# Kernel tuning notes

Measured on AMD Instinct MI355X. Metric: run time of the kernel, lower is better.

Reference implementation:

```python
import jax, jax.numpy as jnp
import numpy as np

B, H, W = 128, 64, 64
MAP = 128          # gff mapping_dim
GFF_SCALE = 10.0   # common default scale for Gaussian Fourier features


def _ku(k, shape, fan_in):
    # torch kaiming_uniform_(a=sqrt(5)) -> bound = 1/sqrt(fan_in)
    b = 1.0 / np.sqrt(fan_in)
    return jax.random.uniform(k, shape, jnp.float32, -b, b)


def setup_inputs() -> dict:
    key = jax.random.key(0)
    ks = jax.random.split(key, 16)
    coords = jax.random.uniform(ks[0], (B, 2, H, W), jnp.float32)
    Bmat = GFF_SCALE * jax.random.normal(ks[1], (2, MAP), jnp.float32)
    # FMMLinear(256, 256_out? no) -- linear1: in=256, out=256, rank=70
    L1 = _ku(ks[2], (256, 70), 70)
    R1 = _ku(ks[3], (70, 256), 256)
    b1 = jax.random.uniform(ks[4], (256,), jnp.float32, -1/np.sqrt(256), 1/np.sqrt(256))
    # linear2: in=256, out=128, rank=10
    L2 = _ku(ks[5], (128, 10), 10)
    R2 = _ku(ks[6], (10, 256), 256)
    b2 = jax.random.uniform(ks[7], (128,), jnp.float32, -1/np.sqrt(256), 1/np.sqrt(256))
    # dense layers (torch nn.Linear default init)
    W3 = _ku(ks[8], (32, 128), 128)
    b3 = jax.random.uniform(ks[9], (32,), jnp.float32, -1/np.sqrt(128), 1/np.sqrt(128))
    W4 = _ku(ks[10], (16, 32), 32)
    b4 = jax.random.uniform(ks[11], (16,), jnp.float32, -1/np.sqrt(32), 1/np.sqrt(32))
    W5 = _ku(ks[12], (3, 16), 16)
    b5 = jax.random.uniform(ks[13], (3,), jnp.float32, -1/np.sqrt(16), 1/np.sqrt(16))
    return dict(coords=coords, Bmat=Bmat, L1=L1, R1=R1, b1=b1,
                L2=L2, R2=R2, b2=b2, W3=W3, b3=b3, W4=W4, b4=b4, W5=W5, b5=b5)


def reference(coords, Bmat, L1, R1, b1, L2, R2, b2, W3, b3, W4, b4, W5, b5):
    # Gaussian Fourier features: [B,2,H,W] -> [B,H,W,2*MAP]
    proj = (2.0 * jnp.pi) * jnp.einsum('bchw,cm->bhwm', coords, Bmat)
    x = jnp.concatenate([jnp.sin(proj), jnp.cos(proj)], axis=-1)
    x = x.reshape(-1, 2 * MAP)                       # (b h w) c
    x = jax.nn.relu(x @ (L1 @ R1).T + b1)            # FMM linear1
    x = jax.nn.relu(x @ (L2 @ R2).T + b2)            # FMM linear2
    x = jax.nn.relu(x @ W3.T + b3)
    x = jax.nn.relu(x @ W4.T + b4)
    out = (x @ W5.T + b5)[None]                      # [1, B*H*W, 3]
    return out
```

## Files before the change

kernel.cpp:

```cpp
#include <hip/hip_runtime.h>


typedef __attribute__((ext_vector_type(8))) short bf16x8;
typedef __attribute__((ext_vector_type(4))) float f32x4;
typedef __attribute__((ext_vector_type(4))) int i32x4;

#define LFENCE() asm volatile("s_waitcnt lgkmcnt(0)" ::: "memory")

__device__ inline unsigned short f2bf(float f) {
  unsigned u = __float_as_uint(f);
  return (unsigned short)((u + 0x7FFFu + ((u >> 16) & 1u)) >> 16);
}

#if __has_builtin(__builtin_amdgcn_cvt_pk_bf16_f32)
typedef __attribute__((ext_vector_type(2))) __bf16 bf16x2;
__device__ inline unsigned pk2bf(float a, float b) {
  bf16x2 v = __builtin_amdgcn_cvt_pk_bf16_f32(a, b);
  return __builtin_bit_cast(unsigned, v);
}
#else
__device__ inline unsigned pk2bf(float a, float b) {
  return ((__float_as_uint(a) + 0x8000u) >> 16) |
         ((__float_as_uint(b) + 0x8000u) & 0xFFFF0000u);
}
#endif

__global__ __launch_bounds__(256) void prep_pack(
    const float* __restrict__ R1, const float* __restrict__ L1,
    const float* __restrict__ R2, const float* __restrict__ L2,
    const float* __restrict__ W3, const float* __restrict__ W4,
    void* __restrict__ ws) {
  unsigned short* w16 = (unsigned short*)ws;
  float* wf = (float*)ws;
  int e = blockIdx.x * 256 + threadIdx.x;
  if (e < 20480) {
    int kt = e / 2560, rem = e % 2560;
    int n = rem >> 5, oj = rem & 31;
    int k = kt * 32 + oj;
    int feat = (k & 1) ? 128 + (k >> 1) : (k >> 1);
    w16[e] = f2bf((n < 70) ? R1[n * 256 + feat] : 0.0f);
  } else if (e < 45056) {
    int f = e - 20480;
    int kt = f / 8192, rem = f % 8192;
    int n = rem >> 5, oj = rem & 31;
    int r = kt * 32 + (oj & 1) * 16 + (oj >> 1);
    w16[e] = f2bf((r < 70) ? L1[n * 70 + r] : 0.0f);
  } else if (e < 49152) {
    int g = e - 45056;
    int rd = g / 512, rem = g % 512;
    int n = rem >> 5, oj = rem & 31;
    int j = rd * 32 + (oj & 1) * 16 + (oj >> 1);
    w16[e] = f2bf((n < 10) ? R2[n * 256 + j] : 0.0f);
  } else if (e < 53248) {
    int f = e - 49152;
    int j = f & 7, h = (f >> 3) & 3, n = (f >> 5) & 15, nt = f >> 9;
    int k = h * 8 + j;
    w16[e] = f2bf((k < 10) ? L2[(nt * 16 + n) * 10 + k] : 0.0f);
  } else if (e < 57344) {
    int f = e - 53248;
    int oj = f & 31, n = (f >> 5) & 15, nt2 = (f >> 9) & 1, rd = f >> 10;
    int i = rd * 32 + (oj & 1) * 16 + (oj >> 1);
    w16[e] = f2bf(W3[(nt2 * 16 + n) * 128 + i]);
  } else if (e < 57856) {
    int h2 = e - 57344;
    int q = h2 >> 4, p = h2 & 15;
    wf[28672 + h2] = W4[p * 32 + q];
  }
}

__global__ __launch_bounds__(128, 2) void mlp_mfma(
    const float* __restrict__ coords, const float* __restrict__ Bm,
    const float* __restrict__ b1, const float* __restrict__ b2,
    const float* __restrict__ b3v, const float* __restrict__ b4v,
    const float* __restrict__ W5, const float* __restrict__ b5,
    const void* __restrict__ ws, float* __restrict__ out) {
  const int l = threadIdx.x & 63;
  const int wv = threadIdx.x >> 6;
  const int lo = l & 15, hi = l >> 4;
  const int pix0 = blockIdx.x * 128 + wv * 64;

  __shared__ __align__(16) char smem[20480];
  char* slice = smem + wv * 10240;
  unsigned short* Y16 = (unsigned short*)slice;
  unsigned short* X16 = (unsigned short*)slice;
  float* O3f = (float*)slice;

  const unsigned short* R1p = (const unsigned short*)ws;
  const unsigned short* L1p = ((const unsigned short*)ws) + 20480;
  const unsigned short* R2p = ((const unsigned short*)ws) + 45056;
  const unsigned short* L2p = ((const unsigned short*)ws) + 49152;
  const unsigned short* W3p = ((const unsigned short*)ws) + 53248;
  const float* W4T = ((const float*)ws) + 28672;

  const f32x4 fz = {0.0f, 0.0f, 0.0f, 0.0f};

  float c0m[4], c1m[4];
#pragma unroll
  for (int mt = 0; mt < 4; ++mt) {
    int p = pix0 + mt * 16 + lo;
    int bb = p >> 12, hw = p & 4095;
    c0m[mt] = coords[bb * 8192 + hw];
    c1m[mt] = coords[bb * 8192 + 4096 + hw];
  }

  f32x4 y[4][5];
#pragma unroll
  for (int mt = 0; mt < 4; ++mt)
#pragma unroll
    for (int nt = 0; nt < 5; ++nt) y[mt][nt] = fz;

  float bm0[4], bm1[4];
#pragma unroll
  for (int p = 0; p < 4; ++p) {
    int m = hi * 4 + p;
    bm0[p] = Bm[m]; bm1[p] = Bm[128 + m];
  }
  for (int kt = 0; kt < 8; ++kt) {
    float nb0[4], nb1[4];
    if (kt < 7) {
#pragma unroll
      for (int p = 0; p < 4; ++p) {
        int m = (kt + 1) * 16 + hi * 4 + p;
        nb0[p] = Bm[m]; nb1[p] = Bm[128 + m];
      }
    }
    bf16x8 bfr[5];
#pragma unroll
    for (int nt = 0; nt < 5; ++nt)
      bfr[nt] = *(const bf16x8*)(R1p + ((kt * 80 + nt * 16 + lo) * 4 + hi) * 8);
    bf16x8 af[4];
#pragma unroll
    for (int mt = 0; mt < 4; ++mt) {
#pragma unroll
      for (int p = 0; p < 4; ++p) {
        float u = fmaf(c0m[mt], bm0[p], c1m[mt] * bm1[p]);
        float t = u - floorf(u);
        float s = __builtin_amdgcn_sinf(t);
        float c = __builtin_amdgcn_cosf(t);
        ((unsigned*)&af[mt])[p] = pk2bf(s, c);
      }
    }
#pragma unroll
    for (int mt = 0; mt < 4; ++mt)
#pragma unroll
      for (int nt = 0; nt < 5; ++nt)
        y[mt][nt] = __builtin_amdgcn_mfma_f32_16x16x32_bf16(af[mt], bfr[nt],
                                                            y[mt][nt], 0, 0, 0);
#pragma unroll
    for (int p = 0; p < 4; ++p) { bm0[p] = nb0[p]; bm1[p] = nb1[p]; }
  }

#pragma unroll
  for (int mt = 0; mt < 4; ++mt)
#pragma unroll
    for (int r = 0; r < 4; ++r) {
      int row = mt * 16 + hi * 4 + r;
      *(unsigned*)(Y16 + row * 72 + lo * 2)      = pk2bf(y[mt][0][r], y[mt][1][r]);
      *(unsigned*)(Y16 + row * 72 + 32 + lo * 2) = pk2bf(y[mt][2][r], y[mt][3][r]);
    }
  LFENCE();
  bf16x8 ay[4][3];
#pragma unroll
  for (int mt = 0; mt < 4; ++mt)
#pragma unroll
    for (int kt = 0; kt < 2; ++kt)
      ay[mt][kt] = *(const bf16x8*)(Y16 + (mt * 16 + lo) * 72 + kt * 32 + hi * 8);
  LFENCE();
#pragma unroll
  for (int mt = 0; mt < 4; ++mt)
#pragma unroll
    for (int r = 0; r < 4; ++r) {
      int row = mt * 16 + hi * 4 + r;
      *(unsigned*)(Y16 + row * 72 + lo * 2) = pk2bf(y[mt][4][r], 0.0f);
    }
  LFENCE();
#pragma unroll
  for (int mt = 0; mt < 4; ++mt)
    ay[mt][2] = *(const bf16x8*)(Y16 + (mt * 16 + lo) * 72 + hi * 8);
  LFENCE();

  f32x4 zfr[4];
#pragma unroll
  for (int mt = 0; mt < 4; ++mt) zfr[mt] = fz;

#pragma unroll
  for (int rd = 0; rd < 8; ++rd) {
    unsigned short* Xb = X16 + (rd & 1) * 2560;
    bf16x8 blE[3], blO[3];
#pragma unroll
    for (int kt = 0; kt < 3; ++kt) {
      blE[kt] = *(const bf16x8*)(L1p + ((kt * 256 + (2 * rd) * 16 + lo) * 4 + hi) * 8);
      blO[kt] = *(const bf16x8*)(L1p + ((kt * 256 + (2 * rd + 1) * 16 + lo) * 4 + hi) * 8);
    }
    float biasE = b1[2 * rd * 16 + lo];
    float biasO = b1[(2 * rd + 1) * 16 + lo];
    f32x4 cfE[4], cfO[4];
#pragma unroll
    for (int mt = 0; mt < 4; ++mt) { cfE[mt] = fz; cfO[mt] = fz; }
#pragma unroll
    for (int kt = 0; kt < 3; ++kt)
#pragma unroll
      for (int mt = 0; mt < 4; ++mt) {
        cfE[mt] = __builtin_amdgcn_mfma_f32_16x16x32_bf16(ay[mt][kt], blE[kt],
                                                          cfE[mt], 0, 0, 0);
        cfO[mt] = __builtin_amdgcn_mfma_f32_16x16x32_bf16(ay[mt][kt], blO[kt],
                                                          cfO[mt], 0, 0, 0);
      }
#pragma unroll
    for (int mt = 0; mt < 4; ++mt)
#pragma unroll
      for (int r = 0; r < 4; ++r) {
        float v0 = fmaxf(cfE[mt][r] + biasE, 0.0f);
        float v1 = fmaxf(cfO[mt][r] + biasO, 0.0f);
        *(unsigned*)(Xb + (mt * 16 + hi * 4 + r) * 40 + lo * 2) = pk2bf(v0, v1);
      }
    LFENCE();
    bf16x8 br = *(const bf16x8*)(R2p + (rd * 16 + lo) * 32 + hi * 8);
#pragma unroll
    for (int mt = 0; mt < 4; ++mt) {
      bf16x8 aa = *(const bf16x8*)(Xb + (mt * 16 + lo) * 40 + hi * 8);
      zfr[mt] = __builtin_amdgcn_mfma_f32_16x16x32_bf16(aa, br, zfr[mt], 0, 0, 0);
    }
  }

  unsigned short* Z16 = X16;
#pragma unroll
  for (int mt = 0; mt < 4; ++mt)
#pragma unroll
    for (int r = 0; r < 4; ++r)
      Z16[(mt * 16 + hi * 4 + r) * 40 + lo] =
          (unsigned short)(pk2bf(zfr[mt][r], 0.0f) & 0xFFFFu);
  *(i32x4*)(Z16 + l * 40 + 16) = (i32x4){0, 0, 0, 0};
  *(i32x4*)(Z16 + l * 40 + 24) = (i32x4){0, 0, 0, 0};
  LFENCE();
  bf16x8 az[4];
#pragma unroll
  for (int mt = 0; mt < 4; ++mt)
    az[mt] = *(const bf16x8*)(Z16 + (mt * 16 + lo) * 40 + hi * 8);
  LFENCE();

  f32x4 o3fr[4][2];
#pragma unroll
  for (int mt = 0; mt < 4; ++mt) { o3fr[mt][0] = fz; o3fr[mt][1] = fz; }

#pragma unroll
  for (int rd = 0; rd < 4; ++rd) {
    unsigned short* Xb = X16 + (rd & 1) * 2560;
    bf16x8 wlE = *(const bf16x8*)(L2p + ((2 * rd) * 16 + lo) * 32 + hi * 8);
    bf16x8 wlO = *(const bf16x8*)(L2p + ((2 * rd + 1) * 16 + lo) * 32 + hi * 8);
    float biasE = b2[2 * rd * 16 + lo];
    float biasO = b2[(2 * rd + 1) * 16 + lo];
    f32x4 cfE[4], cfO[4];
#pragma unroll
    for (int mt = 0; mt < 4; ++mt) {
      cfE[mt] = __builtin_amdgcn_mfma_f32_16x16x32_bf16(az[mt], wlE, fz, 0, 0, 0);
      cfO[mt] = __builtin_amdgcn_mfma_f32_16x16x32_bf16(az[mt], wlO, fz, 0, 0, 0);
    }
#pragma unroll
    for (int mt = 0; mt < 4; ++mt)
#pragma unroll
      for (int r = 0; r < 4; ++r) {
        float v0 = fmaxf(cfE[mt][r] + biasE, 0.0f);
        float v1 = fmaxf(cfO[mt][r] + biasO, 0.0f);
        *(unsigned*)(Xb + (mt * 16 + hi * 4 + r) * 40 + lo * 2) = pk2bf(v0, v1);
      }
    LFENCE();
    bf16x8 bw0 = *(const bf16x8*)(W3p + ((rd * 2 + 0) * 16 + lo) * 32 + hi * 8);
    bf16x8 bw1 = *(const bf16x8*)(W3p + ((rd * 2 + 1) * 16 + lo) * 32 + hi * 8);
#pragma unroll
    for (int mt = 0; mt < 4; ++mt) {
      bf16x8 aa = *(const bf16x8*)(Xb + (mt * 16 + lo) * 40 + hi * 8);
      o3fr[mt][0] = __builtin_amdgcn_mfma_f32_16x16x32_bf16(aa, bw0, o3fr[mt][0],
                                                            0, 0, 0);
      o3fr[mt][1] = __builtin_amdgcn_mfma_f32_16x16x32_bf16(aa, bw1, o3fr[mt][1],
                                                            0, 0, 0);
    }
  }

  LFENCE();
#pragma unroll
  for (int mt = 0; mt < 4; ++mt)
#pragma unroll
    for (int nt2 = 0; nt2 < 2; ++nt2)
#pragma unroll
      for (int r = 0; r < 4; ++r)
        O3f[(mt * 16 + hi * 4 + r) * 33 + nt2 * 16 + lo] =
            fmaxf(o3fr[mt][nt2][r] + b3v[nt2 * 16 + lo], 0.0f);
  LFENCE();

  float o3l[32];
#pragma unroll
  for (int q = 0; q < 32; ++q) o3l[q] = O3f[l * 33 + q];

  float o4[16];
#pragma unroll
  for (int p = 0; p < 16; ++p) o4[p] = b4v[p];
#pragma unroll
  for (int q = 0; q < 32; ++q) {
    float a = o3l[q];
    const float* __restrict__ w4 = W4T + q * 16;
#pragma unroll
    for (int p = 0; p < 16; ++p) o4[p] = fmaf(a, w4[p], o4[p]);
  }
#pragma unroll
  for (int p = 0; p < 16; ++p) o4[p] = fmaxf(o4[p], 0.0f);

#pragma unroll
  for (int e = 0; e < 3; ++e) {
    float acc = b5[e];
    const float* __restrict__ w5 = W5 + e * 16;
#pragma unroll
    for (int p = 0; p < 16; ++p) acc = fmaf(o4[p], w5[p], acc);
    out[(pix0 + l) * 3 + e] = acc;
  }
}

extern "C" void kernel_launch(void* const* d_in, const int* in_sizes, int n_in,
                              void* d_out, int out_size, void* d_ws, size_t ws_size,
                              hipStream_t stream) {
  const float* coords = (const float*)d_in[0];
  const float* Bmat   = (const float*)d_in[1];
  const float* L1     = (const float*)d_in[2];
  const float* R1     = (const float*)d_in[3];
  const float* b1     = (const float*)d_in[4];
  const float* L2     = (const float*)d_in[5];
  const float* R2     = (const float*)d_in[6];
  const float* b2     = (const float*)d_in[7];
  const float* W3     = (const float*)d_in[8];
  const float* b3     = (const float*)d_in[9];
  const float* W4     = (const float*)d_in[10];
  const float* b4     = (const float*)d_in[11];
  const float* W5     = (const float*)d_in[12];
  const float* b5     = (const float*)d_in[13];

  prep_pack<<<227, 256, 0, stream>>>(R1, L1, R2, L2, W3, W4, d_ws);
  mlp_mfma<<<4096, 128, 0, stream>>>(coords, Bmat, b1, b2, b3, b4, W5, b5,
                                     d_ws, (float*)d_out);
}
```

Baseline: 184.9 us.

## Software-pipeline MFMA layer chains, move W4 layer to MFMA, use single-wave blocks

Changes the kernel to one 64-thread wave per block, with more blocks and a smaller shared buffer. The linear1→R2 and L2→W3 chains are software-pipelined: weight fragments and biases for the next round are prefetched, and the previous round's MFMA is issued alongside the current round's. The Y tile is written once with a wider padded stride, which removes one LDS round trip. The fp32 scalar W4 layer becomes a bf16 MFMA fed from a new packed W4 layout, trading some precision and adding register pressure.

```diff
diff --git a/kernel.cpp b/kernel.cpp
--- a/kernel.cpp
+++ b/kernel.cpp
@@ -31,7 +31,6 @@
     const float* __restrict__ W3, const float* __restrict__ W4,
     void* __restrict__ ws) {
   unsigned short* w16 = (unsigned short*)ws;
-  float* wf = (float*)ws;
   int e = blockIdx.x * 256 + threadIdx.x;
   if (e < 20480) {
     int kt = e / 2560, rem = e % 2560;
@@ -53,44 +52,42 @@
     w16[e] = f2bf((n < 10) ? R2[n * 256 + j] : 0.0f);
   } else if (e < 53248) {
     int f = e - 49152;
-    int j = f & 7, h = (f >> 3) & 3, n = (f >> 5) & 15, nt = f >> 9;
-    int k = h * 8 + j;
+    int k = f & 31, n = (f >> 5) & 15, nt = f >> 9;
     w16[e] = f2bf((k < 10) ? L2[(nt * 16 + n) * 10 + k] : 0.0f);
   } else if (e < 57344) {
     int f = e - 53248;
-    int oj = f & 31, n = (f >> 5) & 15, nt2 = (f >> 9) & 1, rd = f >> 10;
+    int oj = f & 31, n = (f >> 5) & 15, s = (f >> 9) & 1, rd = f >> 10;
     int i = rd * 32 + (oj & 1) * 16 + (oj >> 1);
-    w16[e] = f2bf(W3[(nt2 * 16 + n) * 128 + i]);
+    w16[e] = f2bf(W3[(s * 16 + n) * 128 + i]);
   } else if (e < 57856) {
-    int h2 = e - 57344;
-    int q = h2 >> 4, p = h2 & 15;
-    wf[28672 + h2] = W4[p * 32 + q];
-  }
-}
-
-__global__ __launch_bounds__(128, 2) void mlp_mfma(
+    int f = e - 57344;
+    int n = f >> 5, oj = f & 31;
+    int q = (oj & 1) * 16 + (oj >> 1);
+    w16[e] = f2bf(W4[n * 32 + q]);
+  }
+}
+
+__global__ __launch_bounds__(64, 2) void mlp_mfma(
     const float* __restrict__ coords, const float* __restrict__ Bm,
     const float* __restrict__ b1, const float* __restrict__ b2,
     const float* __restrict__ b3v, const float* __restrict__ b4v,
     const float* __restrict__ W5, const float* __restrict__ b5,
     const void* __restrict__ ws, float* __restrict__ out) {
-  const int l = threadIdx.x & 63;
-  const int wv = threadIdx.x >> 6;
+  const int l = threadIdx.x;
   const int lo = l & 15, hi = l >> 4;
-  const int pix0 = blockIdx.x * 128 + wv * 64;
-
-  __shared__ __align__(16) char smem[20480];
-  char* slice = smem + wv * 10240;
-  unsigned short* Y16 = (unsigned short*)slice;
-  unsigned short* X16 = (unsigned short*)slice;
-  float* O3f = (float*)slice;
+  const int pix0 = blockIdx.x * 64;
+
+  __shared__ __align__(16) char smem[13312];
+  unsigned short* Y16 = (unsigned short*)smem;
+  unsigned short* X16 = (unsigned short*)smem;
+  float* O4f = (float*)smem;
 
   const unsigned short* R1p = (const unsigned short*)ws;
   const unsigned short* L1p = ((const unsigned short*)ws) + 20480;
   const unsigned short* R2p = ((const unsigned short*)ws) + 45056;
   const unsigned short* L2p = ((const unsigned short*)ws) + 49152;
   const unsigned short* W3p = ((const unsigned short*)ws) + 53248;
-  const float* W4T = ((const float*)ws) + 28672;
+  const unsigned short* W4p = ((const unsigned short*)ws) + 57344;
 
   const f32x4 fz = {0.0f, 0.0f, 0.0f, 0.0f};
 
@@ -127,7 +124,7 @@
     bf16x8 bfr[5];
 #pragma unroll
     for (int nt = 0; nt < 5; ++nt)
-      bfr[nt] = *(const bf16x8*)(R1p + ((kt * 80 + nt * 16 + lo) * 4 + hi) * 8);
+      bfr[nt] = *(const bf16x8*)(R1p + (kt * 80 + nt * 16 + lo) * 32 + hi * 8);
     bf16x8 af[4];
 #pragma unroll
     for (int mt = 0; mt < 4; ++mt) {
@@ -155,71 +152,84 @@
 #pragma unroll
     for (int r = 0; r < 4; ++r) {
       int row = mt * 16 + hi * 4 + r;
-      *(unsigned*)(Y16 + row * 72 + lo * 2)      = pk2bf(y[mt][0][r], y[mt][1][r]);
-      *(unsigned*)(Y16 + row * 72 + 32 + lo * 2) = pk2bf(y[mt][2][r], y[mt][3][r]);
-    }
+      *(unsigned*)(Y16 + row * 104 + lo * 2)      = pk2bf(y[mt][0][r], y[mt][1][r]);
+      *(unsigned*)(Y16 + row * 104 + 32 + lo * 2) = pk2bf(y[mt][2][r], y[mt][3][r]);
+      *(unsigned*)(Y16 + row * 104 + 64 + lo * 2) = pk2bf(y[mt][4][r], 0.0f);
+    }
+
+  bf16x8 WE[3], WO[3], WEn[3], WOn[3];
+#pragma unroll
+  for (int kt = 0; kt < 3; ++kt) {
+    WE[kt] = *(const bf16x8*)(L1p + (kt * 256 + lo) * 32 + hi * 8);
+    WO[kt] = *(const bf16x8*)(L1p + (kt * 256 + 16 + lo) * 32 + hi * 8);
+  }
+  float bE = b1[lo], bO = b1[16 + lo], bEn, bOn;
+  bf16x8 br_c = *(const bf16x8*)(R2p + lo * 32 + hi * 8);
+  bf16x8 br_u, br_n;
+
   LFENCE();
   bf16x8 ay[4][3];
 #pragma unroll
   for (int mt = 0; mt < 4; ++mt)
 #pragma unroll
-    for (int kt = 0; kt < 2; ++kt)
-      ay[mt][kt] = *(const bf16x8*)(Y16 + (mt * 16 + lo) * 72 + kt * 32 + hi * 8);
-  LFENCE();
-#pragma unroll
-  for (int mt = 0; mt < 4; ++mt)
-#pragma unroll
-    for (int r = 0; r < 4; ++r) {
-      int row = mt * 16 + hi * 4 + r;
-      *(unsigned*)(Y16 + row * 72 + lo * 2) = pk2bf(y[mt][4][r], 0.0f);
-    }
-  LFENCE();
-#pragma unroll
-  for (int mt = 0; mt < 4; ++mt)
-    ay[mt][2] = *(const bf16x8*)(Y16 + (mt * 16 + lo) * 72 + hi * 8);
-  LFENCE();
+    for (int kt = 0; kt < 3; ++kt)
+      ay[mt][kt] = *(const bf16x8*)(Y16 + (mt * 16 + lo) * 104 + kt * 32 + hi * 8);
 
   f32x4 zfr[4];
 #pragma unroll
   for (int mt = 0; mt < 4; ++mt) zfr[mt] = fz;
-
-#pragma unroll
-  for (int rd = 0; rd < 8; ++rd) {
-    unsigned short* Xb = X16 + (rd & 1) * 2560;
-    bf16x8 blE[3], blO[3];
-#pragma unroll
-    for (int kt = 0; kt < 3; ++kt) {
-      blE[kt] = *(const bf16x8*)(L1p + ((kt * 256 + (2 * rd) * 16 + lo) * 4 + hi) * 8);
-      blO[kt] = *(const bf16x8*)(L1p + ((kt * 256 + (2 * rd + 1) * 16 + lo) * 4 + hi) * 8);
-    }
-    float biasE = b1[2 * rd * 16 + lo];
-    float biasO = b1[(2 * rd + 1) * 16 + lo];
+  bf16x8 aa[4];
+
+#pragma unroll
+  for (int rd = 0; rd <= 8; ++rd) {
     f32x4 cfE[4], cfO[4];
-#pragma unroll
-    for (int mt = 0; mt < 4; ++mt) { cfE[mt] = fz; cfO[mt] = fz; }
-#pragma unroll
-    for (int kt = 0; kt < 3; ++kt)
-#pragma unroll
-      for (int mt = 0; mt < 4; ++mt) {
-        cfE[mt] = __builtin_amdgcn_mfma_f32_16x16x32_bf16(ay[mt][kt], blE[kt],
-                                                          cfE[mt], 0, 0, 0);
-        cfO[mt] = __builtin_amdgcn_mfma_f32_16x16x32_bf16(ay[mt][kt], blO[kt],
-                                                          cfO[mt], 0, 0, 0);
-      }
-#pragma unroll
-    for (int mt = 0; mt < 4; ++mt)
-#pragma unroll
-      for (int r = 0; r < 4; ++r) {
-        float v0 = fmaxf(cfE[mt][r] + biasE, 0.0f);
-        float v1 = fmaxf(cfO[mt][r] + biasO, 0.0f);
-        *(unsigned*)(Xb + (mt * 16 + hi * 4 + r) * 40 + lo * 2) = pk2bf(v0, v1);
-      }
-    LFENCE();
-    bf16x8 br = *(const bf16x8*)(R2p + (rd * 16 + lo) * 32 + hi * 8);
-#pragma unroll
-    for (int mt = 0; mt < 4; ++mt) {
-      bf16x8 aa = *(const bf16x8*)(Xb + (mt * 16 + lo) * 40 + hi * 8);
-      zfr[mt] = __builtin_amdgcn_mfma_f32_16x16x32_bf16(aa, br, zfr[mt], 0, 0, 0);
+    if (rd < 8) {
+#pragma unroll
+      for (int mt = 0; mt < 4; ++mt) { cfE[mt] = fz; cfO[mt] = fz; }
+#pragma unroll
+      for (int kt = 0; kt < 3; ++kt)
+#pragma unroll
+        for (int mt = 0; mt < 4; ++mt) {
+          cfE[mt] = __builtin_amdgcn_mfma_f32_16x16x32_bf16(ay[mt][kt], WE[kt],
+                                                            cfE[mt], 0, 0, 0);
+          cfO[mt] = __builtin_amdgcn_mfma_f32_16x16x32_bf16(ay[mt][kt], WO[kt],
+                                                            cfO[mt], 0, 0, 0);
+        }
+    }
+    if (rd > 0) {
+#pragma unroll
+      for (int mt = 0; mt < 4; ++mt)
+        zfr[mt] = __builtin_amdgcn_mfma_f32_16x16x32_bf16(aa[mt], br_u,
+                                                          zfr[mt], 0, 0, 0);
+    }
+    if (rd < 8) {
+      unsigned short* Xb = X16 + (rd & 1) * 2560;
+#pragma unroll
+      for (int mt = 0; mt < 4; ++mt)
+#pragma unroll
+        for (int r = 0; r < 4; ++r) {
+          float v0 = fmaxf(cfE[mt][r] + bE, 0.0f);
+          float v1 = fmaxf(cfO[mt][r] + bO, 0.0f);
+          *(unsigned*)(Xb + (mt * 16 + hi * 4 + r) * 40 + lo * 2) = pk2bf(v0, v1);
+        }
+      if (rd < 7) {
+#pragma unroll
+        for (int kt = 0; kt < 3; ++kt) {
+          WEn[kt] = *(const bf16x8*)(L1p + (kt * 256 + (2 * rd + 2) * 16 + lo) * 32 + hi * 8);
+          WOn[kt] = *(const bf16x8*)(L1p + (kt * 256 + (2 * rd + 3) * 16 + lo) * 32 + hi * 8);
+        }
+        bEn = b1[(2 * rd + 2) * 16 + lo];
+        bOn = b1[(2 * rd + 3) * 16 + lo];
+        br_n = *(const bf16x8*)(R2p + ((rd + 1) * 16 + lo) * 32 + hi * 8);
+      }
+      LFENCE();
+#pragma unroll
+      for (int mt = 0; mt < 4; ++mt)
+        aa[mt] = *(const bf16x8*)(Xb + (mt * 16 + lo) * 40 + hi * 8);
+      br_u = br_c; br_c = br_n;
+#pragma unroll
+      for (int kt = 0; kt < 3; ++kt) { WE[kt] = WEn[kt]; WO[kt] = WOn[kt]; }
+      bE = bEn; bO = bOn;
     }
   }
 
@@ -232,85 +242,110 @@
           (unsigned short)(pk2bf(zfr[mt][r], 0.0f) & 0xFFFFu);
   *(i32x4*)(Z16 + l * 40 + 16) = (i32x4){0, 0, 0, 0};
   *(i32x4*)(Z16 + l * 40 + 24) = (i32x4){0, 0, 0, 0};
+
+  bf16x8 wlE = *(const bf16x8*)(L2p + lo * 32 + hi * 8);
+  bf16x8 wlO = *(const bf16x8*)(L2p + (16 + lo) * 32 + hi * 8);
+  bf16x8 wlEn, wlOn;
+  float cE = b2[lo], cO = b2[16 + lo], cEn, cOn;
+  bf16x8 bw_c0 = *(const bf16x8*)(W3p + lo * 32 + hi * 8);
+  bf16x8 bw_c1 = *(const bf16x8*)(W3p + (16 + lo) * 32 + hi * 8);
+  bf16x8 bw_u0, bw_u1, bw_n0, bw_n1;
+
   LFENCE();
   bf16x8 az[4];
 #pragma unroll
   for (int mt = 0; mt < 4; ++mt)
     az[mt] = *(const bf16x8*)(Z16 + (mt * 16 + lo) * 40 + hi * 8);
+
+  f32x4 o3fr[4][2];
+#pragma unroll
+  for (int mt = 0; mt < 4; ++mt) { o3fr[mt][0] = fz; o3fr[mt][1] = fz; }
+  bf16x8 aaC[4];
+
+#pragma unroll
+  for (int rd = 0; rd <= 4; ++rd) {
+    f32x4 cfE[4], cfO[4];
+    if (rd < 4) {
+#pragma unroll
+      for (int mt = 0; mt < 4; ++mt) {
+        cfE[mt] = __builtin_amdgcn_mfma_f32_16x16x32_bf16(az[mt], wlE, fz, 0, 0, 0);
+        cfO[mt] = __builtin_amdgcn_mfma_f32_16x16x32_bf16(az[mt], wlO, fz, 0, 0, 0);
+      }
+    }
+    if (rd > 0) {
+#pragma unroll
+      for (int mt = 0; mt < 4; ++mt) {
+        o3fr[mt][0] = __builtin_amdgcn_mfma_f32_16x16x32_bf16(aaC[mt], bw_u0,
+                                                              o3fr[mt][0], 0, 0, 0);
+        o3fr[mt][1] = __builtin_amdgcn_mfma_f32_16x16x32_bf16(aaC[mt], bw_u1,
+                                                              o3fr[mt][1], 0, 0, 0);
+      }
+    }
+    if (rd < 4) {
+      unsigned short* Xb = X16 + (rd & 1) * 2560;
+#pragma unroll
+      for (int mt = 0; mt < 4; ++mt)
+#pragma unroll
+        for (int r = 0; r < 4; ++r) {
+          float v0 = fmaxf(cfE[mt][r] + cE, 0.0f);
+          float v1 = fmaxf(cfO[mt][r] + cO, 0.0f);
+          *(unsigned*)(Xb + (mt * 16 + hi * 4 + r) * 40 + lo * 2) = pk2bf(v0, v1);
+        }
+      if (rd < 3) {
+        wlEn = *(const bf16x8*)(L2p + ((2 * rd + 2) * 16 + lo) * 32 + hi * 8);
+        wlOn = *(const bf16x8*)(L2p + ((2 * rd + 3) * 16 + lo) * 32 + hi * 8);
+        cEn = b2[(2 * rd + 2) * 16 + lo];
+        cOn = b2[(2 * rd + 3) * 16 + lo];
+        bw_n0 = *(const bf16x8*)(W3p + ((2 * rd + 2) * 16 + lo) * 32 + hi * 8);
+        bw_n1 = *(const bf16x8*)(W3p + ((2 * rd + 3) * 16 + lo) * 32 + hi * 8);
+      }
+      LFENCE();
+#pragma unroll
+      for (int mt = 0; mt < 4; ++mt)
+        aaC[mt] = *(const bf16x8*)(Xb + (mt * 16 + lo) * 40 + hi * 8);
+      bw_u0 = bw_c0; bw_u1 = bw_c1; bw_c0 = bw_n0; bw_c1 = bw_n1;
+      wlE = wlEn; wlO = wlOn; cE = cEn; cO = cOn;
+    }
+  }
+
+  float b3E = b3v[lo], b3O = b3v[16 + lo];
+  unsigned short* Db = X16;
+#pragma unroll
+  for (int mt = 0; mt < 4; ++mt)
+#pragma unroll
+    for (int r = 0; r < 4; ++r) {
+      float v0 = fmaxf(o3fr[mt][0][r] + b3E, 0.0f);
+      float v1 = fmaxf(o3fr[mt][1][r] + b3O, 0.0f);
+      *(unsigned*)(Db + (mt * 16 + hi * 4 + r) * 40 + lo * 2) = pk2bf(v0, v1);
+    }
+  bf16x8 bw4 = *(const bf16x8*)(W4p + lo * 32 + hi * 8);
+  float b4l = b4v[lo];
   LFENCE();
-
-  f32x4 o3fr[4][2];
-#pragma unroll
-  for (int mt = 0; mt < 4; ++mt) { o3fr[mt][0] = fz; o3fr[mt][1] = fz; }
-
-#pragma unroll
-  for (int rd = 0; rd < 4; ++rd) {
-    unsigned short* Xb = X16 + (rd & 1) * 2560;
-    bf16x8 wlE = *(const bf16x8*)(L2p + ((2 * rd) * 16 + lo) * 32 + hi * 8);
-    bf16x8 wlO = *(const bf16x8*)(L2p + ((2 * rd + 1) * 16 + lo) * 32 + hi * 8);
-    float biasE = b2[2 * rd * 16 + lo];
-    float biasO = b2[(2 * rd + 1) * 16 + lo];
-    f32x4 cfE[4], cfO[4];
-#pragma unroll
-    for (int mt = 0; mt < 4; ++mt) {
-      cfE[mt] = __builtin_amdgcn_mfma_f32_16x16x32_bf16(az[mt], wlE, fz, 0, 0, 0);
-      cfO[mt] = __builtin_amdgcn_mfma_f32_16x16x32_bf16(az[mt], wlO, fz, 0, 0, 0);
-    }
-#pragma unroll
-    for (int mt = 0; mt < 4; ++mt)
-#pragma unroll
-      for (int r = 0; r < 4; ++r) {
-        float v0 = fmaxf(cfE[mt][r] + biasE, 0.0f);
-        float v1 = fmaxf(cfO[mt][r] + biasO, 0.0f);
-        *(unsigned*)(Xb + (mt * 16 + hi * 4 + r) * 40 + lo * 2) = pk2bf(v0, v1);
-      }
-    LFENCE();
-    bf16x8 bw0 = *(const bf16x8*)(W3p + ((rd * 2 + 0) * 16 + lo) * 32 + hi * 8);
-    bf16x8 bw1 = *(const bf16x8*)(W3p + ((rd * 2 + 1) * 16 + lo) * 32 + hi * 8);
-#pragma unroll
-    for (int mt = 0; mt < 4; ++mt) {
-      bf16x8 aa = *(const bf16x8*)(Xb + (mt * 16 + lo) * 40 + hi * 8);
-      o3fr[mt][0] = __builtin_amdgcn_mfma_f32_16x16x32_bf16(aa, bw0, o3fr[mt][0],
-                                                            0, 0, 0);
-      o3fr[mt][1] = __builtin_amdgcn_mfma_f32_16x16x32_bf16(aa, bw1, o3fr[mt][1],
-                                                            0, 0, 0);
-    }
-  }
-
+  bf16x8 aD[4];
+#pragma unroll
+  for (int mt = 0; mt < 4; ++mt)
+    aD[mt] = *(const bf16x8*)(Db + (mt * 16 + lo) * 40 + hi * 8);
+  f32x4 o4fr[4];
+#pragma unroll
+  for (int mt = 0; mt < 4; ++mt)
+    o4fr[mt] = __builtin_amdgcn_mfma_f32_16x16x32_bf16(aD[mt], bw4, fz, 0, 0, 0);
+
+#pragma unroll
+  for (int mt = 0; mt < 4; ++mt)
+#pragma unroll
+    for (int r = 0; r < 4; ++r)
+      O4f[(mt * 16 + hi * 4 + r) * 17 + lo] = fmaxf(o4fr[mt][r] + b4l, 0.0f);
   LFENCE();
-#pragma unroll
-  for (int mt = 0; mt < 4; ++mt)
-#pragma unroll
-    for (int nt2 = 0; nt2 < 2; ++nt2)
-#pragma unroll
-      for (int r = 0; r < 4; ++r)
-        O3f[(mt * 16 + hi * 4 + r) * 33 + nt2 * 16 + lo] =
-            fmaxf(o3fr[mt][nt2][r] + b3v[nt2 * 16 + lo], 0.0f);
-  LFENCE();
-
-  float o3l[32];
-#pragma unroll
-  for (int q = 0; q < 32; ++q) o3l[q] = O3f[l * 33 + q];
-
-  float o4[16];
-#pragma unroll
-  for (int p = 0; p < 16; ++p) o4[p] = b4v[p];
-#pragma unroll
-  for (int q = 0; q < 32; ++q) {
-    float a = o3l[q];
-    const float* __restrict__ w4 = W4T + q * 16;
-#pragma unroll
-    for (int p = 0; p < 16; ++p) o4[p] = fmaf(a, w4[p], o4[p]);
-  }
-#pragma unroll
-  for (int p = 0; p < 16; ++p) o4[p] = fmaxf(o4[p], 0.0f);
+  float o4l[16];
+#pragma unroll
+  for (int q = 0; q < 16; ++q) o4l[q] = O4f[l * 17 + q];
 
 #pragma unroll
   for (int e = 0; e < 3; ++e) {
     float acc = b5[e];
     const float* __restrict__ w5 = W5 + e * 16;
 #pragma unroll
-    for (int p = 0; p < 16; ++p) acc = fmaf(o4[p], w5[p], acc);
+    for (int p = 0; p < 16; ++p) acc = fmaf(o4l[p], w5[p], acc);
     out[(pix0 + l) * 3 + e] = acc;
   }
 }
@@ -334,6 +369,6 @@
   const float* b5     = (const float*)d_in[13];
 
   prep_pack<<<227, 256, 0, stream>>>(R1, L1, R2, L2, W3, W4, d_ws);
-  mlp_mfma<<<4096, 128, 0, stream>>>(coords, Bmat, b1, b2, b3, b4, W5, b5,
-                                     d_ws, (float*)d_out);
-}
+  mlp_mfma<<<8192, 64, 0, stream>>>(coords, Bmat, b1, b2, b3, b4, W5, b5,
+                                    d_ws, (float*)d_out);
+}
```

After: 157.3 us. -15.0%, faster.
